# Kernel optimization log

Measured on AMD Instinct MI355X. Metric: run time of the kernel, lower is better.

The kernel has to match this reference:

```python
import jax, jax.numpy as jnp
import numpy as np

N, E, DIM, H = 50000, 800000, 64, 2
HD = H * DIM


def setup_inputs() -> dict:
    key = jax.random.key(0)
    ks = jax.random.split(key, 16)
    s = 0.05
    return {
        "x": jax.random.normal(ks[0], (N, DIM), jnp.float32),
        "edge_index": jax.random.randint(ks[1], (2, E), 0, N, jnp.int64),
        "Wq": jax.random.normal(ks[2], (DIM, HD), jnp.float32) * s,
        "bq": jax.random.normal(ks[3], (HD,), jnp.float32) * s,
        "Wk": jax.random.normal(ks[4], (DIM, HD), jnp.float32) * s,
        "bk": jax.random.normal(ks[5], (HD,), jnp.float32) * s,
        "Wv": jax.random.normal(ks[6], (DIM, HD), jnp.float32) * s,
        "bv": jax.random.normal(ks[7], (HD,), jnp.float32) * s,
        "Wskip": jax.random.normal(ks[8], (DIM, HD), jnp.float32) * s,
        "bskip": jax.random.normal(ks[9], (HD,), jnp.float32) * s,
        "Wc": jax.random.normal(ks[10], (HD, DIM), jnp.float32) * s,
        "bc": jax.random.normal(ks[11], (DIM,), jnp.float32) * s,
        "gamma": jnp.ones((DIM,), jnp.float32),
        "beta": jnp.zeros((DIM,), jnp.float32),
    }


def reference(x, edge_index, Wq, bq, Wk, bk, Wv, bv, Wskip, bskip, Wc, bc, gamma, beta):
    src, dst = edge_index[0], edge_index[1]  # messages flow src -> dst
    # TransformerConv: per-head q/k/v projections, [N, H, D]
    q = (x @ Wq + bq).reshape(N, H, DIM)
    k = (x @ Wk + bk).reshape(N, H, DIM)
    v = (x @ Wv + bv).reshape(N, H, DIM)
    scale = 1.0 / np.sqrt(DIM).astype(np.float32)
    # edge-wise attention logits: [E, H]
    alpha = jnp.einsum('ehd,ehd->eh', q[dst], k[src]) * scale
    # segment softmax over incoming edges of each dst node (PyG softmax)
    amax = jax.ops.segment_max(alpha, dst, num_segments=N)
    a = jnp.exp(alpha - amax[dst])
    asum = jax.ops.segment_sum(a, dst, num_segments=N)
    a = a / (asum[dst] + 1e-16)
    # weighted scatter-aggregate of values: [N, H, D] -> concat heads
    out = jax.ops.segment_sum(a[:, :, None] * v[src], dst, num_segments=N)
    out = out.reshape(N, HD)
    # root/skip connection (root_weight=True default)
    out = out + (x @ Wskip + bskip)
    # concat linear: H*D -> dim
    out = out @ Wc + bc
    # pyg.LayerNorm default mode='graph': normalize over ALL nodes+features
    out = out - out.mean()
    out = out / (out.std() + 1e-5)  # std with unbiased=False (jnp default ddof=0)
    return out * gamma + beta
```

## Files before the change

### kernel.cpp

```cpp
#include <hip/hip_runtime.h>
#include <hip/hip_bf16.h>

#define N_NODES 50000
#define N_EDGES 800000
#define DIM 64
#define NHEAD 2
#define HD 128
#define NCOL 448
#define MAXDEG 64

#define NBIN 196
#define BCAP 6144
#define ACH 2048
#define BIN_BLKS 391

#define PREP_B 112
#define PROJ_B 782

#define QSCALE 0.18033688011112042f

typedef short bf16x8 __attribute__((ext_vector_type(8)));
typedef float f32x16 __attribute__((ext_vector_type(16)));
typedef float f32x2 __attribute__((ext_vector_type(2)));

__device__ __forceinline__ unsigned short f2bf(float f) {
    unsigned u = __float_as_uint(f);
    unsigned r = (u + 0x7fffu + ((u >> 16) & 1u)) >> 16;
    return (unsigned short)r;
}
__device__ __forceinline__ unsigned char f2fp8(float f) {
    int r = __builtin_amdgcn_cvt_pk_fp8_f32(f, f, 0, false);
    return (unsigned char)(r & 0xff);
}

__global__ __launch_bounds__(256) void k_pb(
    const int* __restrict__ ei,
    const float* __restrict__ Wq, const float* __restrict__ bq,
    const float* __restrict__ Wk, const float* __restrict__ bk,
    const float* __restrict__ Wv, const float* __restrict__ bv,
    const float* __restrict__ Wskip, const float* __restrict__ bskip,
    const float* __restrict__ Wc, const float* __restrict__ bc,
    unsigned short* __restrict__ WallT, float* __restrict__ ball,
    int* __restrict__ bincnt, unsigned* __restrict__ bins,
    double* __restrict__ sacc)
{
    const int t = threadIdx.x;
    if (blockIdx.x < PREP_B) {
        if (blockIdx.x == 0) { sacc[t] = 0.0; sacc[256 + t] = 0.0; }
        int gid = blockIdx.x * 256 + t;
        const int j = gid >> 6;
        const int d = gid & 63;
        float w, bb;
        if (j < 128) {
            w = Wq[d * HD + j] * QSCALE;
            bb = bq[j] * QSCALE;
        } else if (j < 256) {
            int jj = j - 128;
            w = Wk[d * HD + jj];
            bb = bk[jj];
        } else if (j < 384) {
            int jj = j - 256;
            int h = jj >> 6, jc = jj & 63;
            float s = 0.f, sb = 0.f;
            for (int c = 0; c < 64; c++) {
                float wc = Wc[(h * 64 + c) * DIM + jc];
                s  += Wv[d * HD + h * 64 + c] * wc;
                sb += bv[h * 64 + c] * wc;
            }
            w = s; bb = sb;
        } else {
            int jj = j - 384;
            float s = 0.f, sb = bc[jj];
            for (int c = 0; c < HD; c++) {
                float wc = Wc[c * DIM + jj];
                s  += Wskip[d * HD + c] * wc;
                sb += bskip[c] * wc;
            }
            w = s; bb = sb;
        }
        WallT[gid] = f2bf(w);
        if (d == 0) ball[j] = bb;
        return;
    }
    __shared__ int hist[256];
    __shared__ int gbase[256];
    const int e0 = (blockIdx.x - PREP_B) * ACH;
    hist[t] = 0;
    __syncthreads();
    unsigned pk8[8];
    int bin8[8], sl8[8];
#pragma unroll
    for (int k = 0; k < 8; k++) {
        int e = e0 + t + k * 256;
        if (e < N_EDGES) {
            int src = ei[e];
            int d = ei[N_EDGES + e];
            int bin = d >> 8;
            pk8[k] = (unsigned)(((d & 255) << 16) | src);
            bin8[k] = bin;
            sl8[k] = atomicAdd(&hist[bin], 1);
        } else {
            bin8[k] = -1;
        }
    }
    __syncthreads();
    if (t < NBIN) {
        int h = hist[t];
        if (h > 0) gbase[t] = atomicAdd(&bincnt[t], h);
    }
    __syncthreads();
#pragma unroll
    for (int k = 0; k < 8; k++) {
        int bin = bin8[k];
        if (bin >= 0) {
            int pos = gbase[bin] + sl8[k];
            if (pos < BCAP) bins[(size_t)bin * BCAP + pos] = pk8[k];
        }
    }
}

__global__ __launch_bounds__(256) void k_ep(
    const float* __restrict__ x,
    const unsigned short* __restrict__ WallT, const float* __restrict__ ball,
    float* __restrict__ q, unsigned char* __restrict__ kv, float* __restrict__ skipc,
    const int* __restrict__ bincnt, const unsigned* __restrict__ bins,
    int* __restrict__ deg, unsigned short* __restrict__ elist)
{
    const int blk = blockIdx.x;
    const int t = threadIdx.x;
    if (blk >= PROJ_B) {
        const int bin = blk - PROJ_B;
        __shared__ int nodecnt[256];
        nodecnt[t] = 0;
        __syncthreads();
        int cnt = bincnt[bin]; if (cnt > BCAP) cnt = BCAP;
        const unsigned* bp = bins + (size_t)bin * BCAP;
        for (int i = t; i < cnt; i += 256) {
            unsigned p = bp[i];
            int local = p >> 16;
            int src = p & 0xffff;
            int sl = atomicAdd(&nodecnt[local], 1);
            if (sl < MAXDEG)
                elist[((size_t)((bin << 8) | local)) * MAXDEG + sl] = (unsigned short)src;
        }
        __syncthreads();
        int node = (bin << 8) + t;
        if (node < N_NODES) {
            int dgv = nodecnt[t];
            deg[node] = dgv > MAXDEG ? MAXDEG : dgv;
        }
        return;
    }
    const int w = t >> 6;
    const int lane = t & 63;
    const int col = lane & 31;
    const int khalf = lane >> 5;
    const int n0 = blk * 64 + (w >> 1) * 32;
    const int ct0 = (w & 1) * 7;
    const int rowbase = 4 * khalf;

    int nread = n0 + col; if (nread >= N_NODES) nread = N_NODES - 1;
    const float* ap = x + (size_t)nread * 64 + khalf * 8;
    bf16x8 afrag[4];
#pragma unroll
    for (int kk = 0; kk < 4; kk++) {
        float4 xa = *((const float4*)(ap + kk * 16));
        float4 xb4 = *((const float4*)(ap + kk * 16 + 4));
        bf16x8 f;
        f[0] = (short)f2bf(xa.x); f[1] = (short)f2bf(xa.y);
        f[2] = (short)f2bf(xa.z); f[3] = (short)f2bf(xa.w);
        f[4] = (short)f2bf(xb4.x); f[5] = (short)f2bf(xb4.y);
        f[6] = (short)f2bf(xb4.z); f[7] = (short)f2bf(xb4.w);
        afrag[kk] = f;
    }

    for (int tt = 0; tt < 7; tt++) {
        const int gc = (ct0 + tt) * 32 + col;
        const float b = ball[gc];
        f32x16 acc;
#pragma unroll
        for (int r = 0; r < 16; r++) acc[r] = b;
        const unsigned short* bp = WallT + (size_t)gc * 64 + khalf * 8;
#pragma unroll
        for (int kk = 0; kk < 4; kk++) {
            bf16x8 bfrag = *((const bf16x8*)(bp + kk * 16));
            acc = __builtin_amdgcn_mfma_f32_32x32x16_bf16(afrag[kk], bfrag, acc, 0, 0, 0);
        }
        if (gc < 128) {
#pragma unroll
            for (int r = 0; r < 16; r++) {
                int node = n0 + (r & 3) + 8 * (r >> 2) + rowbase;
                if (node < N_NODES) q[(size_t)node * HD + gc] = acc[r];
            }
        } else if (gc < 384) {
            int ch = gc - 128;
            int half = ch >> 7;
            int cc = ch & 127;
            int h = cc >> 6, c = cc & 63;
            int pos = half * 128 + ((c >> 3) << 4) + (h << 3) + (c & 7);
#pragma unroll
            for (int r = 0; r < 16; r++) {
                int node = n0 + (r & 3) + 8 * (r >> 2) + rowbase;
                if (node < N_NODES) kv[(size_t)node * 256 + pos] = f2fp8(acc[r]);
            }
        } else {
#pragma unroll
            for (int r = 0; r < 16; r++) {
                int node = n0 + (r & 3) + 8 * (r >> 2) + rowbase;
                if (node < N_NODES) skipc[(size_t)node * DIM + (gc - 384)] = acc[r];
            }
        }
    }
}

__global__ __launch_bounds__(256) void k_attn(
    const float* __restrict__ q, const unsigned char* __restrict__ kv,
    const float* __restrict__ skipc,
    const int* __restrict__ deg, const unsigned short* __restrict__ elist,
    float* __restrict__ out, double* __restrict__ sacc)
{
    const int w = threadIdx.x >> 6;
    const int lane = threadIdx.x & 63;
    const int g = lane >> 3;
    const int j = lane & 7;
    const int n = blockIdx.x * 4 + w;
    const f32x2* qp = (const f32x2*)(q + (size_t)n * HD);
    f32x2 q0[4], q1[4];
#pragma unroll
    for (int i = 0; i < 4; i++) { q0[i] = qp[4 * j + i]; q1[i] = qp[32 + 4 * j + i]; }
    const int myE = elist[(size_t)n * MAXDEG + lane];
    f32x2 acc0[4], acc1[4];
#pragma unroll
    for (int i = 0; i < 4; i++) {
        acc0[i] = (f32x2){0.f, 0.f};
        acc1[i] = (f32x2){0.f, 0.f};
    }
    float l0 = 0.f, l1 = 0.f;
    int dg = deg[n]; if (dg > MAXDEG) dg = MAXDEG;
    for (int b0 = 0; b0 < dg; b0 += 8) {
        int idx = b0 + g;
        bool valid = idx < dg;
        int s = __shfl(myE, valid ? idx : 0, 64);
        const uint4* kp = (const uint4*)(kv + (size_t)s * 256);
        uint4 K = kp[j];
        uint4 V = kp[8 + j];
        f32x2 p0v = q0[0] * __builtin_amdgcn_cvt_pk_f32_fp8(K.x, false);
        p0v += q0[1] * __builtin_amdgcn_cvt_pk_f32_fp8(K.x, true);
        p0v += q0[2] * __builtin_amdgcn_cvt_pk_f32_fp8(K.y, false);
        p0v += q0[3] * __builtin_amdgcn_cvt_pk_f32_fp8(K.y, true);
        f32x2 p1v = q1[0] * __builtin_amdgcn_cvt_pk_f32_fp8(K.z, false);
        p1v += q1[1] * __builtin_amdgcn_cvt_pk_f32_fp8(K.z, true);
        p1v += q1[2] * __builtin_amdgcn_cvt_pk_f32_fp8(K.w, false);
        p1v += q1[3] * __builtin_amdgcn_cvt_pk_f32_fp8(K.w, true);
        float p0 = p0v[0] + p0v[1];
        float p1 = p1v[0] + p1v[1];
#pragma unroll
        for (int off = 1; off < 8; off <<= 1) {
            p0 += __shfl_xor(p0, off, 64);
            p1 += __shfl_xor(p1, off, 64);
        }
        float w0 = valid ? __builtin_amdgcn_exp2f(p0) : 0.f;
        float w1 = valid ? __builtin_amdgcn_exp2f(p1) : 0.f;
        l0 += w0; l1 += w1;
        f32x2 w0v = {w0, w0}, w1v = {w1, w1};
        acc0[0] += w0v * __builtin_amdgcn_cvt_pk_f32_fp8(V.x, false);
        acc0[1] += w0v * __builtin_amdgcn_cvt_pk_f32_fp8(V.x, true);
        acc0[2] += w0v * __builtin_amdgcn_cvt_pk_f32_fp8(V.y, false);
        acc0[3] += w0v * __builtin_amdgcn_cvt_pk_f32_fp8(V.y, true);
        acc1[0] += w1v * __builtin_amdgcn_cvt_pk_f32_fp8(V.z, false);
        acc1[1] += w1v * __builtin_amdgcn_cvt_pk_f32_fp8(V.z, true);
        acc1[2] += w1v * __builtin_amdgcn_cvt_pk_f32_fp8(V.w, false);
        acc1[3] += w1v * __builtin_amdgcn_cvt_pk_f32_fp8(V.w, true);
    }
    float* a0 = (float*)acc0;
    float* a1 = (float*)acc1;
#pragma unroll
    for (int off = 8; off < 64; off <<= 1) {
        l0 += __shfl_xor(l0, off, 64);
        l1 += __shfl_xor(l1, off, 64);
#pragma unroll
        for (int i = 0; i < 8; i++) {
            a0[i] += __shfl_xor(a0[i], off, 64);
            a1[i] += __shfl_xor(a1[i], off, 64);
        }
    }
    if (g == 0) {
        float inv0 = 1.f / (l0 + 1e-16f), inv1 = 1.f / (l1 + 1e-16f);
        const float4* sk = (const float4*)(skipc + (size_t)n * DIM);
        float4 sa = sk[2 * j], sb = sk[2 * j + 1];
        float o[8];
        o[0] = a0[0] * inv0 + a1[0] * inv1 + sa.x;
        o[1] = a0[1] * inv0 + a1[1] * inv1 + sa.y;
        o[2] = a0[2] * inv0 + a1[2] * inv1 + sa.z;
        o[3] = a0[3] * inv0 + a1[3] * inv1 + sa.w;
        o[4] = a0[4] * inv0 + a1[4] * inv1 + sb.x;
        o[5] = a0[5] * inv0 + a1[5] * inv1 + sb.y;
        o[6] = a0[6] * inv0 + a1[6] * inv1 + sb.z;
        o[7] = a0[7] * inv0 + a1[7] * inv1 + sb.w;
        float4 r0 = {o[0], o[1], o[2], o[3]}, r1 = {o[4], o[5], o[6], o[7]};
        float4* op = (float4*)(out + (size_t)n * DIM);
        op[2 * j] = r0; op[2 * j + 1] = r1;
        float s_ = 0.f, ss = 0.f;
#pragma unroll
        for (int i = 0; i < 8; i++) { s_ += o[i]; ss += o[i] * o[i]; }
#pragma unroll
        for (int off = 1; off < 8; off <<= 1) {
            s_ += __shfl_xor(s_, off, 64);
            ss += __shfl_xor(ss, off, 64);
        }
        if (j == 0) {
            int slot = n & 255;
            atomicAdd(&sacc[slot], (double)s_);
            atomicAdd(&sacc[256 + slot], (double)ss);
        }
    }
}

__global__ __launch_bounds__(256) void k_norm(
    float* __restrict__ out, const double* __restrict__ sacc,
    const float* __restrict__ gamma, const float* __restrict__ beta)
{
    const int t = threadIdx.x;
    __shared__ double red[8];
    double s = sacc[t];
    double ss = sacc[256 + t];
#pragma unroll
    for (int off = 32; off > 0; off >>= 1) {
        s  += __shfl_down(s, off);
        ss += __shfl_down(ss, off);
    }
    int wv = t >> 6;
    if ((t & 63) == 0) { red[wv * 2] = s; red[wv * 2 + 1] = ss; }
    __syncthreads();
    double S  = red[0] + red[2] + red[4] + red[6];
    double SS = red[1] + red[3] + red[5] + red[7];
    const double cnt = (double)N_NODES * (double)DIM;
    double mean = S / cnt;
    double var  = SS / cnt - mean * mean;
    if (var < 0.0) var = 0.0;
    float mf = (float)mean;
    float inv = 1.0f / ((float)sqrt(var) + 1e-5f);
    int i = blockIdx.x * 256 + t;
    if (i >= N_NODES * DIM / 4) return;
    float4 v = ((const float4*)out)[i];
    float4 gv = ((const float4*)gamma)[i & 15];
    float4 bv2 = ((const float4*)beta)[i & 15];
    v.x = (v.x - mf) * inv * gv.x + bv2.x;
    v.y = (v.y - mf) * inv * gv.y + bv2.y;
    v.z = (v.z - mf) * inv * gv.z + bv2.z;
    v.w = (v.w - mf) * inv * gv.w + bv2.w;
    ((float4*)out)[i] = v;
}

extern "C" void kernel_launch(void* const* d_in, const int* in_sizes, int n_in,
                              void* d_out, int out_size, void* d_ws, size_t ws_size,
                              hipStream_t stream) {
    const float* x     = (const float*)d_in[0];
    const int*   ei    = (const int*)d_in[1];
    const float* Wq    = (const float*)d_in[2];
    const float* bq    = (const float*)d_in[3];
    const float* Wk    = (const float*)d_in[4];
    const float* bk    = (const float*)d_in[5];
    const float* Wv    = (const float*)d_in[6];
    const float* bv    = (const float*)d_in[7];
    const float* Wsk   = (const float*)d_in[8];
    const float* bsk   = (const float*)d_in[9];
    const float* Wc    = (const float*)d_in[10];
    const float* bc    = (const float*)d_in[11];
    const float* gamma = (const float*)d_in[12];
    const float* beta  = (const float*)d_in[13];
    float* out = (float*)d_out;

    double* sacc = (double*)d_ws;
    float* ws = (float*)(sacc + 512);
    const size_t NF = (size_t)N_NODES * HD;
    float* q = ws;
    unsigned char* kv = (unsigned char*)(ws + NF);
    float* skipc = (float*)(kv + (size_t)N_NODES * 256);
    unsigned short* WallT = (unsigned short*)(skipc + (size_t)N_NODES * DIM);
    float* ball   = (float*)(WallT + NCOL * 64);
    int* bincnt   = (int*)(ball + NCOL);
    unsigned* bins = (unsigned*)(bincnt + 256);
    int* deg      = (int*)(bins + (size_t)NBIN * BCAP);
    unsigned short* elist = (unsigned short*)(deg + N_NODES);

    hipMemsetAsync(bincnt, 0, 256 * sizeof(int), stream);
    hipLaunchKernelGGL(k_pb, dim3(PREP_B + BIN_BLKS), dim3(256), 0, stream,
                       ei, Wq, bq, Wk, bk, Wv, bv, Wsk, bsk, Wc, bc,
                       WallT, ball, bincnt, bins, sacc);
    hipLaunchKernelGGL(k_ep, dim3(PROJ_B + NBIN), dim3(256), 0, stream,
                       x, WallT, ball, q, kv, skipc, bincnt, bins, deg, elist);
    hipLaunchKernelGGL(k_attn, dim3(N_NODES / 4), dim3(256), 0, stream,
                       q, kv, skipc, deg, elist, out, sacc);
    hipLaunchKernelGGL(k_norm, dim3(N_NODES * DIM / 4 / 256 + 1), dim3(256), 0, stream,
                       out, sacc, gamma, beta);
}
```

Measured before the change: 185.7 us.

## Stage projection outputs in LDS for coalesced stores; vectorize q and skip loads

The projection kernel now writes its MFMA results for q, the fp8 k/v block and the skip term into a 64KB shared-memory tile. After a barrier it copies each tile to global memory with contiguous 16-byte stores, replacing scattered per-element stores (including single-byte fp8 writes). The attention kernel loads q with float4 reads and issues the skip load before the edge loop so its latency is hidden. The 64KB of LDS per block reduces occupancy for both the projection and the binning blocks, and LDS bank conflicts on the staging writes may add cost.

```diff
diff --git a/kernel.cpp b/kernel.cpp
--- a/kernel.cpp
+++ b/kernel.cpp
@@ -126,11 +126,12 @@
     const int* __restrict__ bincnt, const unsigned* __restrict__ bins,
     int* __restrict__ deg, unsigned short* __restrict__ elist)
 {
+    __shared__ __align__(16) unsigned char smem[65536];
     const int blk = blockIdx.x;
     const int t = threadIdx.x;
     if (blk >= PROJ_B) {
         const int bin = blk - PROJ_B;
-        __shared__ int nodecnt[256];
+        int* nodecnt = (int*)smem;
         nodecnt[t] = 0;
         __syncthreads();
         int cnt = bincnt[bin]; if (cnt > BCAP) cnt = BCAP;
@@ -151,11 +152,16 @@
         }
         return;
     }
+    float* q_s = (float*)smem;
+    unsigned char* kv_s = smem + 32768;
+    float* sk_s = (float*)(smem + 49152);
+
     const int w = t >> 6;
     const int lane = t & 63;
     const int col = lane & 31;
     const int khalf = lane >> 5;
-    const int n0 = blk * 64 + (w >> 1) * 32;
+    const int nloc0 = (w >> 1) * 32;
+    const int n0 = blk * 64 + nloc0;
     const int ct0 = (w & 1) * 7;
     const int rowbase = 4 * khalf;
 
@@ -189,8 +195,8 @@
         if (gc < 128) {
 #pragma unroll
             for (int r = 0; r < 16; r++) {
-                int node = n0 + (r & 3) + 8 * (r >> 2) + rowbase;
-                if (node < N_NODES) q[(size_t)node * HD + gc] = acc[r];
+                int nl = nloc0 + rowbase + (r & 3) + 8 * (r >> 2);
+                q_s[nl * 128 + gc] = acc[r];
             }
         } else if (gc < 384) {
             int ch = gc - 128;
@@ -200,15 +206,49 @@
             int pos = half * 128 + ((c >> 3) << 4) + (h << 3) + (c & 7);
 #pragma unroll
             for (int r = 0; r < 16; r++) {
-                int node = n0 + (r & 3) + 8 * (r >> 2) + rowbase;
-                if (node < N_NODES) kv[(size_t)node * 256 + pos] = f2fp8(acc[r]);
+                int nl = nloc0 + rowbase + (r & 3) + 8 * (r >> 2);
+                kv_s[nl * 256 + pos] = f2fp8(acc[r]);
             }
         } else {
+            int c = gc - 384;
 #pragma unroll
             for (int r = 0; r < 16; r++) {
-                int node = n0 + (r & 3) + 8 * (r >> 2) + rowbase;
-                if (node < N_NODES) skipc[(size_t)node * DIM + (gc - 384)] = acc[r];
+                int nl = nloc0 + rowbase + (r & 3) + 8 * (r >> 2);
+                sk_s[nl * 64 + c] = acc[r];
             }
+        }
+    }
+    __syncthreads();
+    const size_t nbase = (size_t)blk * 64;
+    const int nrem = (int)(N_NODES - nbase);
+    {
+        const float4* s4 = (const float4*)q_s;
+        float4* g4 = (float4*)(q + nbase * HD);
+        int lim = nrem >= 64 ? 2048 : nrem * 32;
+#pragma unroll
+        for (int kk = 0; kk < 8; kk++) {
+            int i = t + kk * 256;
+            if (i < lim) g4[i] = s4[i];
+        }
+    }
+    {
+        const uint4* s4 = (const uint4*)kv_s;
+        uint4* g4 = (uint4*)(kv + nbase * 256);
+        int lim = nrem >= 64 ? 1024 : nrem * 16;
+#pragma unroll
+        for (int kk = 0; kk < 4; kk++) {
+            int i = t + kk * 256;
+            if (i < lim) g4[i] = s4[i];
+        }
+    }
+    {
+        const float4* s4 = (const float4*)sk_s;
+        float4* g4 = (float4*)(skipc + nbase * DIM);
+        int lim = nrem >= 64 ? 1024 : nrem * 16;
+#pragma unroll
+        for (int kk = 0; kk < 4; kk++) {
+            int i = t + kk * 256;
+            if (i < lim) g4[i] = s4[i];
         }
     }
 }
@@ -224,11 +264,20 @@
     const int g = lane >> 3;
     const int j = lane & 7;
     const int n = blockIdx.x * 4 + w;
-    const f32x2* qp = (const f32x2*)(q + (size_t)n * HD);
+    const float4* qp4 = (const float4*)(q + (size_t)n * HD);
+    const float4 qa = qp4[2 * j],      qb = qp4[2 * j + 1];
+    const float4 qc = qp4[16 + 2 * j], qd = qp4[17 + 2 * j];
     f32x2 q0[4], q1[4];
-#pragma unroll
-    for (int i = 0; i < 4; i++) { q0[i] = qp[4 * j + i]; q1[i] = qp[32 + 4 * j + i]; }
+    q0[0] = (f32x2){qa.x, qa.y}; q0[1] = (f32x2){qa.z, qa.w};
+    q0[2] = (f32x2){qb.x, qb.y}; q0[3] = (f32x2){qb.z, qb.w};
+    q1[0] = (f32x2){qc.x, qc.y}; q1[1] = (f32x2){qc.z, qc.w};
+    q1[2] = (f32x2){qd.x, qd.y}; q1[3] = (f32x2){qd.z, qd.w};
     const int myE = elist[(size_t)n * MAXDEG + lane];
+    float4 sa = {0,0,0,0}, sb = {0,0,0,0};
+    if (g == 0) {
+        const float4* sk = (const float4*)(skipc + (size_t)n * DIM);
+        sa = sk[2 * j]; sb = sk[2 * j + 1];
+    }
     f32x2 acc0[4], acc1[4];
 #pragma unroll
     for (int i = 0; i < 4; i++) {
@@ -286,8 +335,6 @@
     }
     if (g == 0) {
         float inv0 = 1.f / (l0 + 1e-16f), inv1 = 1.f / (l1 + 1e-16f);
-        const float4* sk = (const float4*)(skipc + (size_t)n * DIM);
-        float4 sa = sk[2 * j], sb = sk[2 * j + 1];
         float o[8];
         o[0] = a0[0] * inv0 + a1[0] * inv1 + sa.x;
         o[1] = a0[1] * inv0 + a1[1] * inv1 + sa.y;
```

After: 187.1 us. No clear change (+0.7%).
